# Optimization experiments

Measured on AMD Instinct MI355X. Metric: run time of the kernel, lower is better.

The kernel has to match this reference:

```python
import math
import jax, jax.numpy as jnp
import numpy as np

B, S, D, H = 4, 1024, 512, 8
DK = D // H


def lin(x, W, b):
    # torch nn.Linear: y = x @ W.T + b, W: [out, in]
    return jnp.einsum('...i,oi->...o', x, W) + b


def layer_norm(x, scale, bias, eps=1e-5):
    m = jnp.mean(x, axis=-1, keepdims=True)
    v = jnp.var(x, axis=-1, keepdims=True)
    return (x - m) / jnp.sqrt(v + eps) * scale + bias


def mha(q_in, k_in, v_in, Wq, bq, Wk, bk, Wv, bv, Wo, bo, gammas, mask, zero_pad):
    b, s, _ = q_in.shape
    q = lin(q_in, Wq, bq).reshape(b, s, H, DK).transpose(0, 2, 1, 3)  # bhsd
    k = lin(k_in, Wk, bk).reshape(b, s, H, DK).transpose(0, 2, 1, 3)
    v = lin(v_in, Wv, bv).reshape(b, s, H, DK).transpose(0, 2, 1, 3)
    scores = jnp.einsum('bhid,bhjd->bhij', q, k) / math.sqrt(DK)
    # no-grad distance-decay branch
    s_ = jnp.where(mask, scores, jnp.float32(-1e32))
    s_ = jax.nn.softmax(s_, axis=-1) * mask
    distcum = jnp.cumsum(s_, axis=-1)
    disttotal = jnp.sum(s_, axis=-1, keepdims=True)
    idx = jnp.arange(s)
    pos = jnp.abs(idx[None, :] - idx[:, None]).astype(jnp.float32)[None, None]  # |i-j|
    dist = jax.lax.stop_gradient(jnp.sqrt(jnp.clip((disttotal - distcum) * pos, 0.0, None)))
    gamma = -jax.nn.softplus(gammas)[None]  # [1,h,1,1]
    total_effect = jnp.clip(jnp.exp(dist * gamma), 1e-5, 1e5)
    scores = scores * total_effect
    # NOTE: original code calls scores.masked_fill(...) without assignment (no-op);
    # faithfully NOT re-masking before this softmax.
    att = jax.nn.softmax(scores, axis=-1)
    if zero_pad:
        att = att.at[:, :, 0, :].set(0.0)
    out = jnp.einsum('bhij,bhjd->bhid', att, v).transpose(0, 2, 1, 3).reshape(b, s, D)
    return lin(out, Wo, bo)


def setup_inputs() -> dict:
    key = jax.random.key(0)
    ks = jax.random.split(key, 32)
    ki = iter(range(32))

    def w(shape, scale=0.02):
        return jax.random.normal(ks[next(ki)], shape, jnp.float32) * scale

    inp = {
        'q_emb': jax.random.normal(ks[next(ki)], (B, S, D), jnp.float32),
        'qa_emb': jax.random.normal(ks[next(ki)], (B, S, D), jnp.float32),
    }
    for blk in (1, 2, 3):
        inp[f'Wq{blk}'] = w((D, D)); inp[f'bq{blk}'] = jnp.zeros((D,), jnp.float32)
        if blk == 3:
            inp['Wk3'] = w((D, D)); inp['bk3'] = jnp.zeros((D,), jnp.float32)
        inp[f'Wv{blk}'] = w((D, D)); inp[f'bv{blk}'] = jnp.zeros((D,), jnp.float32)
        inp[f'Wo{blk}'] = w((D, D)); inp[f'bo{blk}'] = jnp.zeros((D,), jnp.float32)
        inp[f'g{blk}'] = w((H, 1, 1), 0.5)
        inp[f'ls{blk}'] = jnp.ones((D,), jnp.float32)
        inp[f'lb{blk}'] = jnp.zeros((D,), jnp.float32)
    inp['know'] = jax.random.uniform(ks[next(ki)], (1, 1, D), jnp.float32, -1.0, 1.0)
    inp['Wlk'] = w((D, DK)); inp['b_lk'] = jnp.zeros((D,), jnp.float32)
    inp['Wlv'] = w((D, DK)); inp['b_lv'] = jnp.zeros((D,), jnp.float32)
    return inp


def reference(q_emb, qa_emb,
              Wq1, bq1, Wv1, bv1, Wo1, bo1, g1, ls1, lb1,
              Wq2, bq2, Wv2, bv2, Wo2, bo2, g2, ls2, lb2,
              Wq3, bq3, Wk3, bk3, Wv3, bv3, Wo3, bo3, g3, ls3, lb3,
              know, Wlk, b_lk, Wlv, b_lv):
    b, s, d = q_emb.shape
    ones = jnp.ones((s, s), dtype=bool)
    mask_peek = jnp.tril(ones, k=0)[None, None]   # peek_cur=True
    mask_nopeek = jnp.tril(ones, k=-1)[None, None]  # peek_cur=False

    # block1 / block2 share k and q projections (kq_same=True)
    hq = layer_norm(q_emb + mha(q_emb, q_emb, q_emb, Wq1, bq1, Wq1, bq1,
                                Wv1, bv1, Wo1, bo1, g1, mask_peek, False), ls1, lb1)
    ha = layer_norm(qa_emb + mha(qa_emb, qa_emb, qa_emb, Wq2, bq2, Wq2, bq2,
                                 Wv2, bv2, Wo2, bo2, g2, mask_peek, False), ls2, lb2)
    query = jnp.broadcast_to(know, (b, s, d))
    h = layer_norm(query + mha(query, hq, ha, Wq3, bq3, Wk3, bk3,
                               Wv3, bv3, Wo3, bo3, g3, mask_nopeek, True), ls3, lb3)

    # small multi-head combine
    key_t = jax.nn.sigmoid(lin(query.reshape(b, s, H, DK), Wlk, b_lk))  # [b,s,h,d]
    val_t = jax.nn.sigmoid(lin(h.reshape(b, s, H, DK), Wlv, b_lv))     # [b,s,h,d]
    beta = jnp.einsum('bshd,bsd->bsh', key_t, q_emb)
    alpha = jax.nn.softmax(beta, axis=-1)
    out = jnp.einsum('bsh,bshd->bsd', alpha, val_t)
    return out
```

## Files before the change

### kernel.cpp

```cpp
#include <hip/hip_runtime.h>
#include <math.h>

#define BB 4
#define S 1024
#define D 512
#define H 8
#define DKH 64

#define ATT_LD 1032
#define LOG2E 1.4426950408889634f

typedef __attribute__((ext_vector_type(8))) short bf16x8;
typedef __attribute__((ext_vector_type(4))) float f32x4;

#if __has_builtin(__builtin_amdgcn_exp2f)
#define EXP2(x) __builtin_amdgcn_exp2f(x)
#else
#define EXP2(x) exp2f(x)
#endif
#if __has_builtin(__builtin_amdgcn_sqrtf)
#define SQRTF(x) __builtin_amdgcn_sqrtf(x)
#else
#define SQRTF(x) sqrtf(x)
#endif
#if __has_builtin(__builtin_amdgcn_rcpf)
#define RCPF(x) __builtin_amdgcn_rcpf(x)
#else
#define RCPF(x) (1.0f / (x))
#endif

__device__ __forceinline__ unsigned short f2bf(float f){
  unsigned int u = __float_as_uint(f);
  u += 0x7FFFu + ((u >> 16) & 1u);
  return (unsigned short)(u >> 16);
}
__device__ __forceinline__ unsigned short f2bf_rhu(float f){
  return (unsigned short)((__float_as_uint(f) + 0x8000u) >> 16);
}
__device__ __forceinline__ unsigned int pk_rhu(float lo, float hi){
  unsigned int a = __float_as_uint(lo) + 0x8000u;
  unsigned int b = __float_as_uint(hi) + 0x8000u;
#if __has_builtin(__builtin_amdgcn_perm)
  return __builtin_amdgcn_perm(b, a, 0x07060302u);
#else
  return (a >> 16) | (b & 0xffff0000u);
#endif
}
__device__ __forceinline__ float bf2f(unsigned int v){
  return __uint_as_float(v << 16);
}
__device__ __forceinline__ f32x4 MFMA(bf16x8 a, bf16x8 b, f32x4 c){
  return __builtin_amdgcn_mfma_f32_16x16x32_bf16(a, b, c, 0, 0, 0);
}
__device__ __forceinline__ void gl_lds16(const void* g, void* l){
  __builtin_amdgcn_global_load_lds(
      (const __attribute__((address_space(1))) void*)g,
      (__attribute__((address_space(3))) void*)l, 16, 0, 0);
}

template<int CTRL>
__device__ __forceinline__ float dppadd(float v){
  int s = __builtin_amdgcn_update_dpp(0, __float_as_int(v), CTRL, 0xf, 0xf, true);
  return v + __int_as_float(s);
}
__device__ __forceinline__ float rdl(float v, int l){
  return __int_as_float(__builtin_amdgcn_readlane(__float_as_int(v), l));
}
__device__ __forceinline__ void wave_scan64(float v, int lane, float& incl, float& total){
  float r = dppadd<0x111>(v);
  r = dppadd<0x112>(r);
  r = dppadd<0x114>(r);
  r = dppadd<0x118>(r);
  float t0 = rdl(r, 15), t1 = rdl(r, 31), t2 = rdl(r, 47), t3 = rdl(r, 63);
  const int row = lane >> 4;
  float off = (row > 0 ? t0 : 0.f) + (row > 1 ? t1 : 0.f) + (row > 2 ? t2 : 0.f);
  incl = r + off;
  total = (t0 + t1) + (t2 + t3);
}
__device__ __forceinline__ float wave_sum64(float v){
  float r = dppadd<0x111>(v);
  r = dppadd<0x112>(r);
  r = dppadd<0x114>(r);
  r = dppadd<0x118>(r);
  return (rdl(r, 15) + rdl(r, 31)) + (rdl(r, 47) + rdl(r, 63));
}

__device__ __forceinline__ float blk_sum(float* r, int t, float v){
  r[t] = v; __syncthreads();
  for (int s = 128; s > 0; s >>= 1){
    if (t < s) r[t] += r[t + s];
    __syncthreads();
  }
  float res = r[0]; __syncthreads();
  return res;
}

struct GemmJobs {
  const unsigned short* A[4];
  const unsigned short* W[4];
  const float* bias[4];
  void* C[4];
};
template<int OUTBF>
__global__ __launch_bounds__(256) void mfma_gemm_b(GemmJobs jb)
{
  __shared__ __align__(16) short As[128][32];
  __shared__ __align__(16) short Ws[128][32];
  const int t = threadIdx.x;
  const int z = blockIdx.z;
  const int n0 = blockIdx.x * 128, m0 = blockIdx.y * 128;
  const unsigned short* A = jb.A[z];
  const unsigned short* W = jb.W[z];
  const float* bias = jb.bias[z];
  const int w = t >> 6, lane = t & 63;
  const int wm = (w >> 1) << 6, wn = (w & 1) << 6;
  const int lm = lane & 15, q = lane >> 4;
  const int r = t >> 2, cc = (t & 3) << 3;
  char* ldsA = ((char*)&As[0][0]) + w * 1024;
  char* ldsW = ((char*)&Ws[0][0]) + w * 1024;
  f32x4 acc[4][4];
  #pragma unroll
  for (int a_ = 0; a_ < 4; a_++)
    #pragma unroll
    for (int b_ = 0; b_ < 4; b_++)
      acc[a_][b_] = (f32x4){0.f, 0.f, 0.f, 0.f};
  for (int k0 = 0; k0 < D; k0 += 32){
    gl_lds16(&A[(size_t)(m0 + r)      * D + k0 + cc], ldsA);
    gl_lds16(&A[(size_t)(m0 + r + 64) * D + k0 + cc], ldsA + 4096);
    gl_lds16(&W[(size_t)(n0 + r)      * D + k0 + cc], ldsW);
    gl_lds16(&W[(size_t)(n0 + r + 64) * D + k0 + cc], ldsW + 4096);
    __syncthreads();
    bf16x8 af[4], bf[4];
    #pragma unroll
    for (int mt = 0; mt < 4; mt++) af[mt] = *(const bf16x8*)&As[wm + mt*16 + lm][q*8];
    #pragma unroll
    for (int nt = 0; nt < 4; nt++) bf[nt] = *(const bf16x8*)&Ws[wn + nt*16 + lm][q*8];
    #pragma unroll
    for (int mt = 0; mt < 4; mt++)
      #pragma unroll
      for (int nt = 0; nt < 4; nt++)
        acc[mt][nt] = MFMA(af[mt], bf[nt], acc[mt][nt]);
    __syncthreads();
  }
  #pragma unroll
  for (int nt = 0; nt < 4; nt++){
    const int n = n0 + wn + nt*16 + lm;
    const float bs = bias[n];
    #pragma unroll
    for (int mt = 0; mt < 4; mt++){
      const int mb = m0 + wm + mt*16 + (q << 2);
      f32x4 c = acc[mt][nt];
      #pragma unroll
      for (int rr = 0; rr < 4; rr++){
        float vv = c[rr] + bs;
        if (OUTBF)
          ((unsigned short*)jb.C[z])[(size_t)(mb + rr) * D + n] = f2bf(vv);
        else
          ((float*)jb.C[z])[(size_t)(mb + rr) * D + n] = vv;
      }
    }
  }
}

#define KS_LD 66
struct VTArgs { const unsigned short* v[2]; unsigned short* vt[2]; };
__global__ __launch_bounds__(256) void vt_kernel(VTArgs a)
{
  __shared__ unsigned short tile[64 * KS_LD];
  const int z = blockIdx.z, bh = blockIdx.y, b = bh >> 3, h = bh & 7;
  const int j0 = blockIdx.x * 64;
  const int t = threadIdx.x;
  const unsigned short* vp = a.v[z];
  unsigned short* vtp = a.vt[z] + (size_t)bh * 64 * S;
  #pragma unroll
  for (int p = 0; p < 2; p++){
    int lin = t + p * 256, row = lin >> 3, c8 = (lin & 7) << 3;
    *(uint4*)&tile[row * KS_LD + c8] =
      *(const uint4*)&vp[((size_t)b * S + j0 + row) * D + h * DKH + c8];
  }
  __syncthreads();
  #pragma unroll
  for (int p = 0; p < 2; p++){
    int lin = t + p * 256, d = lin >> 3, c8 = (lin & 7) << 3;
    unsigned short tmp[8];
    #pragma unroll
    for (int jx = 0; jx < 8; jx++) tmp[jx] = tile[(c8 + jx) * KS_LD + d];
    *(uint4*)&vtp[(size_t)d * S + j0 + c8] = *(const uint4*)tmp;
  }
}

struct FAArgs {
  const unsigned short* qk[2];
  const unsigned short* vt[2];
  unsigned short* ctx[2];
  const float* g[2];
  const float* c3;
  int diag, zero_pad;
};
template<int C3>
__global__ __launch_bounds__(256, 4) void fused_attn(FAArgs a)
{
  __shared__ __align__(16) unsigned short att[16 * ATT_LD];
  __shared__ float ls2s[16];
  const int t = threadIdx.x;
  const int z = blockIdx.z;
  const int bh = blockIdx.y, b = bh >> 3, h = bh & 7;
  const int i0 = blockIdx.x * 16;
  const int w = t >> 6, lane = t & 63, lm = lane & 15, q = lane >> 4;
  const unsigned short* qkp = a.qk[z];
  const unsigned short* vtp = a.vt[z] + (size_t)bh * 64 * S;
  unsigned short* ctxp = a.ctx[z];
  float gm2;
  { float gv = a.g[z][h];
    gm2 = -((gv > 20.f) ? gv : log1pf(expf(gv))) * LOG2E; }

  if (!C3){
    const size_t rowbase = (size_t)b * S;
    bf16x8 af0 = *(const bf16x8*)&qkp[(rowbase + i0 + lm) * D + h * DKH + q*8];
    bf16x8 af1 = *(const bf16x8*)&qkp[(rowbase + i0 + lm) * D + h * DKH + 32 + q*8];
    size_t kb = (rowbase + w*16 + lm) * D + h * DKH;
    bf16x8 bv0 = *(const bf16x8*)&qkp[kb + q*8];
    bf16x8 bv1 = *(const bf16x8*)&qkp[kb + 32 + q*8];
    for (int jc = 0; jc < S; jc += 64){
      bf16x8 nb0, nb1;
      if (jc + 64 < S){
        size_t kb2 = (rowbase + jc + 64 + w*16 + lm) * D + h * DKH;
        nb0 = *(const bf16x8*)&qkp[kb2 + q*8];
        nb1 = *(const bf16x8*)&qkp[kb2 + 32 + q*8];
      }
      f32x4 acc = (f32x4){0.f, 0.f, 0.f, 0.f};
      acc = MFMA(af0, bv0, acc);
      acc = MFMA(af1, bv1, acc);
      #pragma unroll
      for (int rr = 0; rr < 4; rr++)
        att[(q*4 + rr) * ATT_LD + jc + w*16 + lm] = f2bf_rhu(acc[rr] * 0.125f);
      bv0 = nb0; bv1 = nb1;
    }
  }
  __syncthreads();

  const int jA0 = lane * 8, jB0 = 512 + lane * 8;

  float cH[16], erH[16];
  if (C3){
    const float* c3p = a.c3 + ((size_t)b * H + h) * S;
    #pragma unroll
    for (int sg = 0; sg < 2; sg++)
      #pragma unroll
      for (int p4 = 0; p4 < 2; p4++){
        float4 x = *(const float4*)&c3p[sg*512 + lane*8 + p4*4];
        cH[sg*8+p4*4+0] = x.x * LOG2E; cH[sg*8+p4*4+1] = x.y * LOG2E;
        cH[sg*8+p4*4+2] = x.z * LOG2E; cH[sg*8+p4*4+3] = x.w * LOG2E;
      }
    #pragma unroll
    for (int k = 0; k < 16; k++) erH[k] = EXP2(cH[k]);
  }

  auto decay_row = [&](const float (&c)[16], const float (&er)[16],
                       const int i, unsigned short* rowp, const int rl){
    const int jmax = i + a.diag;
    const bool skipB = (jmax < 512);
    float pl[16];
    float runA = 0.f;
    #pragma unroll
    for (int k = 0; k < 8; k++){
      float e = (jA0 + k <= jmax) ? er[k] : 0.f;
      runA += e; pl[k] = runA;
    }
    float sA, TA;
    wave_scan64(runA, lane, sA, TA);
    float T = TA, sB = 0.f, runB = 0.f;
    if (!skipB){
      #pragma unroll
      for (int k = 0; k < 8; k++){
        float e = (jB0 + k <= jmax) ? er[8+k] : 0.f;
        runB += e; pl[8+k] = runB;
      }
      float TB;
      wave_scan64(runB, lane, sB, TB);
      T = TA + TB;
    }
    const float inv1 = RCPF(T);
    const float cbaseA = (T - (sA - runA)) * inv1;
    const float fiA = (float)(i - jA0);
    float ls2 = 0.f;
    #pragma unroll
    for (int k = 0; k < 8; k++){
      float remn = fmaf(-pl[k], inv1, cbaseA);
      float pos  = fabsf(fiA - (float)k);
      float dist = SQRTF(fmaxf(remn * pos, 0.f));
      float eff  = fmaxf(EXP2(gm2 * dist), 1e-5f);
      float pp   = EXP2(c[k] * eff);
      ls2 += pp; pl[k] = pp;
    }
    if (!skipB){
      const float cbaseB = (T - (TA + sB - runB)) * inv1;
      const float fiB = (float)(i - jB0);
      #pragma unroll
      for (int k = 0; k < 8; k++){
        float remn = fmaf(-pl[8+k], inv1, cbaseB);
        float pos  = fabsf(fiB - (float)k);
        float dist = SQRTF(fmaxf(remn * pos, 0.f));
        float eff  = fmaxf(EXP2(gm2 * dist), 1e-5f);
        float pp   = EXP2(c[8+k] * eff);
        ls2 += pp; pl[8+k] = pp;
      }
    } else {
      #pragma unroll
      for (int k = 0; k < 8; k++){ pl[8+k] = er[8+k]; ls2 += er[8+k]; }
    }
    ls2 = wave_sum64(ls2);
    if (lane == 0) ls2s[rl] = RCPF(ls2);
    #pragma unroll
    for (int sg = 0; sg < 2; sg++){
      uint4 o;
      o.x = pk_rhu(pl[sg*8+0], pl[sg*8+1]);
      o.y = pk_rhu(pl[sg*8+2], pl[sg*8+3]);
      o.z = pk_rhu(pl[sg*8+4], pl[sg*8+5]);
      o.w = pk_rhu(pl[sg*8+6], pl[sg*8+7]);
      *(uint4*)&rowp[sg*512 + lane*8] = o;
    }
  };

  for (int rloc = 0; rloc < 4; rloc++){
    const int rl = w*4 + rloc;
    const int i = i0 + rl;
    unsigned short* rowp = &att[rl * ATT_LD];
    if (C3 && a.zero_pad && i == 0){
      uint4 zz = make_uint4(0u,0u,0u,0u);
      *(uint4*)&rowp[jA0] = zz;
      *(uint4*)&rowp[jB0] = zz;
      if (lane == 0) ls2s[0] = 1.f;
      continue;
    }
    if (C3){
      decay_row(cH, erH, i, rowp, rl);
    } else {
      float c[16], er[16];
      #pragma unroll
      for (int sg = 0; sg < 2; sg++){
        uint4 u = *(const uint4*)&rowp[sg*512 + lane*8];
        unsigned int uu[4] = {u.x, u.y, u.z, u.w};
        #pragma unroll
        for (int mel = 0; mel < 4; mel++){
          c[sg*8 + mel*2]     = bf2f(uu[mel] & 0xffffu) * LOG2E;
          c[sg*8 + mel*2 + 1] = bf2f(uu[mel] >> 16) * LOG2E;
        }
      }
      #pragma unroll
      for (int k = 0; k < 16; k++) er[k] = EXP2(c[k]);
      decay_row(c, er, i, rowp, rl);
    }
  }
  __syncthreads();

  f32x4 acc = (f32x4){0.f,0.f,0.f,0.f};
  const unsigned short* vrow = &vtp[(size_t)(w*16 + lm) * S];
  bf16x8 bv0 = *(const bf16x8*)&vrow[q*8];
  bf16x8 bv1 = *(const bf16x8*)&vrow[32 + q*8];
  for (int kc = 0; kc < S; kc += 64){
    bf16x8 nb0, nb1;
    if (kc + 64 < S){
      nb0 = *(const bf16x8*)&vrow[kc + 64 + q*8];
      nb1 = *(const bf16x8*)&vrow[kc + 96 + q*8];
    }
    bf16x8 a0 = *(const bf16x8*)&att[lm * ATT_LD + kc + q*8];
    bf16x8 a1 = *(const bf16x8*)&att[lm * ATT_LD + kc + 32 + q*8];
    acc = MFMA(a0, bv0, acc);
    acc = MFMA(a1, bv1, acc);
    bv0 = nb0; bv1 = nb1;
  }
  #pragma unroll
  for (int rr = 0; rr < 4; rr++){
    const int rl = q*4 + rr;
    const float sc = ls2s[rl];
    const int row = i0 + rl;
    ctxp[((size_t)b * S + row) * D + h * DKH + w*16 + lm] = f2bf(acc[rr] * sc);
  }
}

struct LNJobs {
  const float* resid[2];
  const float* y[2];
  const float* ls[2];
  const float* lb[2];
  unsigned short* out[2];
  int bcast[2];
};
__global__ __launch_bounds__(256) void ln_residual_b(LNJobs j)
{
  const int z = blockIdx.y;
  const int r = blockIdx.x, t = threadIdx.x;
  __shared__ float red[256];
  const size_t base = (size_t)r * D;
  const float* resid = j.resid[z];
  const float* y = j.y[z];
  const int bcast = j.bcast[z];
  float r0 = bcast ? resid[t]       : resid[base + t];
  float r1 = bcast ? resid[t + 256] : resid[base + t + 256];
  float x0 = r0 + y[base + t];
  float x1 = r1 + y[base + t + 256];
  float mean = blk_sum(red, t, x0 + x1) * (1.0f / 512.0f);
  float d0 = x0 - mean, d1 = x1 - mean;
  float var = blk_sum(red, t, d0*d0 + d1*d1) * (1.0f / 512.0f);
  float inv = rsqrtf(var + 1e-5f);
  j.out[z][base + t]       = f2bf(d0 * inv * j.ls[z][t]       + j.lb[z][t]);
  j.out[z][base + t + 256] = f2bf(d1 * inv * j.ls[z][t + 256] + j.lb[z][t + 256]);
}

struct CvtJobs {
  const float* s[12];
  unsigned short* d[12];
  int n[12];
};
__global__ __launch_bounds__(256) void cvt_all(CvtJobs jb){
  const int z = blockIdx.y;
  const int n = jb.n[z];
  const float* s = jb.s[z];
  unsigned short* d = jb.d[z];
  for (int idx = blockIdx.x * 256 + threadIdx.x; idx < n; idx += gridDim.x * 256)
    d[idx] = f2bf(s[idx]);
}

__global__ __launch_bounds__(256) void know_kernel(
    const float* __restrict__ know, const float* __restrict__ Wq3,
    const float* __restrict__ bq3, float* __restrict__ q3,
    const float* __restrict__ Wlk, const float* __restrict__ blk_,
    float* __restrict__ keyt)
{
  if (blockIdx.x < 128){
    const int wv = (blockIdx.x * 256 + threadIdx.x) >> 6;
    const int lane = threadIdx.x & 63;
    const float* wr = Wq3 + (size_t)wv * 512 + lane * 8;
    const float* kr = know + lane * 8;
    float4 w0 = *(const float4*)&wr[0], w1 = *(const float4*)&wr[4];
    float4 k0 = *(const float4*)&kr[0], k1 = *(const float4*)&kr[4];
    float p = w0.x*k0.x + w0.y*k0.y + w0.z*k0.z + w0.w*k0.w
            + w1.x*k1.x + w1.y*k1.y + w1.z*k1.z + w1.w*k1.w;
    p = wave_sum64(p);
    if (lane == 0) q3[wv] = p + bq3[wv];
  } else {
    int idx = (blockIdx.x - 128) * 256 + threadIdx.x;
    int h = idx >> 9, n = idx & 511;
    float acc = 0.f;
    for (int i = 0; i < 64; i++) acc += know[h * 64 + i] * Wlk[(size_t)n * 64 + i];
    keyt[idx] = 1.f / (1.f + __expf(-(acc + blk_[n])));
  }
}

__global__ __launch_bounds__(256) void scores3_kernel(
    const float* __restrict__ q3, const unsigned short* __restrict__ k3,
    float* __restrict__ c3)
{
  int idx = blockIdx.x * 256 + threadIdx.x;
  int j  = idx & (S - 1);
  int bh = idx >> 10;
  int h  = bh & 7, b = bh >> 3;
  const unsigned short* kp = k3 + ((size_t)b * S + j) * D + h * DKH;
  const float* qp = q3 + h * DKH;
  float acc = 0.f;
  #pragma unroll
  for (int d8 = 0; d8 < 64; d8 += 8){
    uint4 u = *(const uint4*)&kp[d8];
    unsigned int uu[4] = {u.x, u.y, u.z, u.w};
    #pragma unroll
    for (int mel = 0; mel < 4; mel++){
      acc += qp[d8 + 2*mel]     * bf2f(uu[mel] & 0xffffu);
      acc += qp[d8 + 2*mel + 1] * bf2f(uu[mel] >> 16);
    }
  }
  c3[idx] = acc * 0.125f;
}

__global__ __launch_bounds__(256) void alphas_kernel(
    const float* __restrict__ keyt, const float* __restrict__ q_emb,
    float* __restrict__ alpha)
{
  const int row = blockIdx.x * 4 + (threadIdx.x >> 6);
  const int l = threadIdx.x & 63;
  const int h = l >> 3, sub = l & 7;
  const float* qr = q_emb + (size_t)row * D;
  const float* kt = keyt + h * D;
  float p = 0.f;
  for (int d = sub; d < D; d += 8) p += kt[d] * qr[d];
  p += __shfl_xor(p, 1, 64);
  p += __shfl_xor(p, 2, 64);
  p += __shfl_xor(p, 4, 64);
  float m = p;
  m = fmaxf(m, __shfl_xor(m, 8, 64));
  m = fmaxf(m, __shfl_xor(m, 16, 64));
  m = fmaxf(m, __shfl_xor(m, 32, 64));
  float e = __expf(p - m);
  float ssum = e;
  ssum += __shfl_xor(ssum, 8, 64);
  ssum += __shfl_xor(ssum, 16, 64);
  ssum += __shfl_xor(ssum, 32, 64);
  if (sub == 0) alpha[(size_t)row * H + h] = e / ssum;
}

__global__ __launch_bounds__(256) void val_fused(
    const unsigned short* __restrict__ Ah,
    const unsigned short* __restrict__ Wv,
    const float* __restrict__ blv,
    const float* __restrict__ alpha,
    float* __restrict__ out)
{
  __shared__ __align__(16) short As[128][32];
  __shared__ __align__(16) short Ws[128][32];
  __shared__ float als[128];
  const int t = threadIdx.x;
  const int n0 = blockIdx.x * 128, m0 = blockIdx.y * 128;
  if (t < 128) als[t] = alpha[m0 + t];
  const int w = t >> 6, lane = t & 63;
  const int wm = (w >> 1) << 6, wn = (w & 1) << 6;
  const int lm = lane & 15, q = lane >> 4;
  const int r = t >> 2, cc = (t & 3) << 3;
  f32x4 acc[4][4];
  #pragma unroll
  for (int a_ = 0; a_ < 4; a_++)
    #pragma unroll
    for (int b_ = 0; b_ < 4; b_++)
      acc[a_][b_] = (f32x4){0.f, 0.f, 0.f, 0.f};
  for (int k0 = 0; k0 < 64; k0 += 32){
    *(uint4*)&As[r][cc]      = *(const uint4*)&Ah[(size_t)(m0 + r) * 64 + k0 + cc];
    *(uint4*)&As[r + 64][cc] = *(const uint4*)&Ah[(size_t)(m0 + r + 64) * 64 + k0 + cc];
    *(uint4*)&Ws[r][cc]      = *(const uint4*)&Wv[(size_t)(n0 + r) * 64 + k0 + cc];
    *(uint4*)&Ws[r + 64][cc] = *(const uint4*)&Wv[(size_t)(n0 + r + 64) * 64 + k0 + cc];
    __syncthreads();
    bf16x8 af[4], bf[4];
    #pragma unroll
    for (int mt = 0; mt < 4; mt++) af[mt] = *(const bf16x8*)&As[wm + mt*16 + lm][q*8];
    #pragma unroll
    for (int nt = 0; nt < 4; nt++) bf[nt] = *(const bf16x8*)&Ws[wn + nt*16 + lm][q*8];
    #pragma unroll
    for (int mt = 0; mt < 4; mt++)
      #pragma unroll
      for (int nt = 0; nt < 4; nt++)
        acc[mt][nt] = MFMA(af[mt], bf[nt], acc[mt][nt]);
    __syncthreads();
  }
  #pragma unroll
  for (int nt = 0; nt < 4; nt++){
    const int n = n0 + wn + nt*16 + lm;
    const float bs = blv[n];
    #pragma unroll
    for (int mt = 0; mt < 4; mt++){
      const int mb = m0 + wm + mt*16;
      f32x4 c = acc[mt][nt];
      float part = 0.f;
      #pragma unroll
      for (int rr = 0; rr < 4; rr++){
        const int ml = (mb - m0) + (q << 2) + rr;
        float sg = 1.f / (1.f + __expf(-(c[rr] + bs)));
        part += als[ml] * sg;
      }
      part += __shfl_xor(part, 16, 64);
      if ((q & 1) == 0){
        const int srow = (mb >> 3) + (q >> 1);
        out[(size_t)srow * D + n] = part;
      }
    }
  }
}

extern "C" void kernel_launch(void* const* d_in, const int* in_sizes, int n_in,
                              void* d_out, int out_size, void* d_ws, size_t ws_size,
                              hipStream_t stream) {
  const float* q_emb  = (const float*)d_in[0];
  const float* qa_emb = (const float*)d_in[1];
  const float* Wq1 = (const float*)d_in[2],  *bq1 = (const float*)d_in[3];
  const float* Wv1 = (const float*)d_in[4],  *bv1 = (const float*)d_in[5];
  const float* Wo1 = (const float*)d_in[6],  *bo1 = (const float*)d_in[7];
  const float* g1  = (const float*)d_in[8],  *ls1 = (const float*)d_in[9],  *lb1 = (const float*)d_in[10];
  const float* Wq2 = (const float*)d_in[11], *bq2 = (const float*)d_in[12];
  const float* Wv2 = (const float*)d_in[13], *bv2 = (const float*)d_in[14];
  const float* Wo2 = (const float*)d_in[15], *bo2 = (const float*)d_in[16];
  const float* g2  = (const float*)d_in[17], *ls2 = (const float*)d_in[18], *lb2 = (const float*)d_in[19];
  const float* Wq3 = (const float*)d_in[20], *bq3 = (const float*)d_in[21];
  const float* Wk3 = (const float*)d_in[22], *bk3 = (const float*)d_in[23];
  const float* Wv3 = (const float*)d_in[24], *bv3 = (const float*)d_in[25];
  const float* Wo3 = (const float*)d_in[26], *bo3 = (const float*)d_in[27];
  const float* g3  = (const float*)d_in[28], *ls3 = (const float*)d_in[29], *lb3 = (const float*)d_in[30];
  const float* know = (const float*)d_in[31];
  const float* Wlk  = (const float*)d_in[32], *b_lk = (const float*)d_in[33];
  const float* Wlv  = (const float*)d_in[34], *b_lv = (const float*)d_in[35];
  float* outp = (float*)d_out;

  const size_t NSD = (size_t)BB * S * D;
  unsigned short* p = (unsigned short*)d_ws;
  unsigned short* qk1b = p; p += NSD;
  unsigned short* v1b  = p; p += NSD;
  unsigned short* qk2b = p; p += NSD;
  unsigned short* v2b  = p; p += NSD;
  unsigned short* k3b  = p; p += NSD;
  unsigned short* v3b  = p; p += NSD;
  unsigned short* ctx1b= p; p += NSD;
  unsigned short* ctx2b= p; p += NSD;
  unsigned short* ctx3b= p; p += NSD;
  unsigned short* xqb  = p; p += NSD;
  unsigned short* xab  = p; p += NSD;
  unsigned short* hqb  = p; p += NSD;
  unsigned short* hab  = p; p += NSD;
  unsigned short* hfb  = p; p += NSD;
  unsigned short* vt1  = p; p += NSD;
  unsigned short* vt2  = p; p += NSD;
  unsigned short* vt3  = p; p += NSD;
  unsigned short* wb   = p; p += (size_t)9 * D * D;
  unsigned short* wlvb = p; p += (size_t)D * DKH;
  float* yv0   = (float*)p;
  float* yv1   = yv0 + NSD;
  float* q3    = yv1 + NSD;
  float* keyt  = q3 + 512;
  float* c3    = keyt + 4096;
  float* alpha = c3 + (size_t)BB * H * S;

  unsigned short* Wq1b = wb + 0*(size_t)D*D;
  unsigned short* Wv1b = wb + 1*(size_t)D*D;
  unsigned short* Wo1b = wb + 2*(size_t)D*D;
  unsigned short* Wq2b = wb + 3*(size_t)D*D;
  unsigned short* Wv2b = wb + 4*(size_t)D*D;
  unsigned short* Wo2b = wb + 5*(size_t)D*D;
  unsigned short* Wk3b = wb + 6*(size_t)D*D;
  unsigned short* Wv3b = wb + 7*(size_t)D*D;
  unsigned short* Wo3b = wb + 8*(size_t)D*D;

  CvtJobs jb;
  jb.s[0] = q_emb;  jb.d[0] = xqb;  jb.n[0] = (int)NSD;
  jb.s[1] = qa_emb; jb.d[1] = xab;  jb.n[1] = (int)NSD;
  jb.s[2] = Wq1; jb.d[2] = Wq1b; jb.n[2] = D*D;
  jb.s[3] = Wv1; jb.d[3] = Wv1b; jb.n[3] = D*D;
  jb.s[4] = Wo1; jb.d[4] = Wo1b; jb.n[4] = D*D;
  jb.s[5] = Wq2; jb.d[5] = Wq2b; jb.n[5] = D*D;
  jb.s[6] = Wv2; jb.d[6] = Wv2b; jb.n[6] = D*D;
  jb.s[7] = Wo2; jb.d[7] = Wo2b; jb.n[7] = D*D;
  jb.s[8] = Wk3; jb.d[8] = Wk3b; jb.n[8] = D*D;
  jb.s[9] = Wv3; jb.d[9] = Wv3b; jb.n[9] = D*D;
  jb.s[10] = Wo3; jb.d[10] = Wo3b; jb.n[10] = D*D;
  jb.s[11] = Wlv; jb.d[11] = wlvb; jb.n[11] = D*DKH;
  cvt_all<<<dim3(256, 12), 256, 0, stream>>>(jb);

  {
    GemmJobs g;
    g.A[0]=xqb; g.W[0]=Wq1b; g.bias[0]=bq1; g.C[0]=qk1b;
    g.A[1]=xqb; g.W[1]=Wv1b; g.bias[1]=bv1; g.C[1]=v1b;
    g.A[2]=xab; g.W[2]=Wq2b; g.bias[2]=bq2; g.C[2]=qk2b;
    g.A[3]=xab; g.W[3]=Wv2b; g.bias[3]=bv2; g.C[3]=v2b;
    mfma_gemm_b<1><<<dim3(4, 32, 4), 256, 0, stream>>>(g);
  }
  { VTArgs a; a.v[0]=v1b; a.v[1]=v2b; a.vt[0]=vt1; a.vt[1]=vt2;
    vt_kernel<<<dim3(16, 32, 2), 256, 0, stream>>>(a); }
  { FAArgs a;
    a.qk[0]=qk1b; a.qk[1]=qk2b; a.vt[0]=vt1; a.vt[1]=vt2;
    a.ctx[0]=ctx1b; a.ctx[1]=ctx2b; a.g[0]=g1; a.g[1]=g2;
    a.c3=nullptr; a.diag=0; a.zero_pad=0;
    fused_attn<0><<<dim3(64, 32, 2), 256, 0, stream>>>(a); }
  {
    GemmJobs g;
    g.A[0]=ctx1b; g.W[0]=Wo1b; g.bias[0]=bo1; g.C[0]=yv0;
    g.A[1]=ctx2b; g.W[1]=Wo2b; g.bias[1]=bo2; g.C[1]=yv1;
    g.A[2]=ctx1b; g.W[2]=Wo1b; g.bias[2]=bo1; g.C[2]=yv0;
    g.A[3]=ctx1b; g.W[3]=Wo1b; g.bias[3]=bo1; g.C[3]=yv0;
    mfma_gemm_b<0><<<dim3(4, 32, 2), 256, 0, stream>>>(g);
  }
  {
    LNJobs lj;
    lj.resid[0]=q_emb;  lj.y[0]=yv0; lj.ls[0]=ls1; lj.lb[0]=lb1; lj.out[0]=hqb; lj.bcast[0]=0;
    lj.resid[1]=qa_emb; lj.y[1]=yv1; lj.ls[1]=ls2; lj.lb[1]=lb2; lj.out[1]=hab; lj.bcast[1]=0;
    ln_residual_b<<<dim3(BB*S, 2), 256, 0, stream>>>(lj);
  }

  know_kernel<<<144, 256, 0, stream>>>(know, Wq3, bq3, q3, Wlk, b_lk, keyt);
  {
    GemmJobs g;
    g.A[0]=hqb; g.W[0]=Wk3b; g.bias[0]=bk3; g.C[0]=k3b;
    g.A[1]=hab; g.W[1]=Wv3b; g.bias[1]=bv3; g.C[1]=v3b;
    g.A[2]=hqb; g.W[2]=Wk3b; g.bias[2]=bk3; g.C[2]=k3b;
    g.A[3]=hqb; g.W[3]=Wk3b; g.bias[3]=bk3; g.C[3]=k3b;
    mfma_gemm_b<1><<<dim3(4, 32, 2), 256, 0, stream>>>(g);
  }
  { VTArgs a; a.v[0]=v3b; a.v[1]=v3b; a.vt[0]=vt3; a.vt[1]=vt3;
    vt_kernel<<<dim3(16, 32, 1), 256, 0, stream>>>(a); }
  scores3_kernel<<<128, 256, 0, stream>>>(q3, k3b, c3);
  { FAArgs a;
    a.qk[0]=k3b; a.qk[1]=k3b; a.vt[0]=vt3; a.vt[1]=vt3;
    a.ctx[0]=ctx3b; a.ctx[1]=ctx3b; a.g[0]=g3; a.g[1]=g3;
    a.c3=c3; a.diag=-1; a.zero_pad=1;
    fused_attn<1><<<dim3(64, 32, 1), 256, 0, stream>>>(a); }
  {
    GemmJobs g;
    g.A[0]=ctx3b; g.W[0]=Wo3b; g.bias[0]=bo3; g.C[0]=yv0;
    g.A[1]=ctx3b; g.W[1]=Wo3b; g.bias[1]=bo3; g.C[1]=yv0;
    g.A[2]=ctx3b; g.W[2]=Wo3b; g.bias[2]=bo3; g.C[2]=yv0;
    g.A[3]=ctx3b; g.W[3]=Wo3b; g.bias[3]=bo3; g.C[3]=yv0;
    mfma_gemm_b<0><<<dim3(4, 32, 1), 256, 0, stream>>>(g);
  }
  {
    LNJobs lj;
    lj.resid[0]=know; lj.y[0]=yv0; lj.ls[0]=ls3; lj.lb[0]=lb3; lj.out[0]=hfb; lj.bcast[0]=1;
    lj.resid[1]=know; lj.y[1]=yv0; lj.ls[1]=ls3; lj.lb[1]=lb3; lj.out[1]=hfb; lj.bcast[1]=1;
    ln_residual_b<<<dim3(BB*S, 1), 256, 0, stream>>>(lj);
  }

  alphas_kernel<<<1024, 256, 0, stream>>>(keyt, q_emb, alpha);
  val_fused<<<dim3(4, 256), 256, 0, stream>>>(hfb, wlvb, b_lv, alpha, outp);
}
```

Measured before the change: 430.3 us.

## Double fused attention block to 512 threads with split-K PV reduction

The fused attention kernel now runs 8 waves per block instead of 4. Each wave handles two score rows instead of four, the QK score tiles are strided across 8 waves, and the P·V product is split along the key dimension, with the two halves combined through shared memory. The softmax normalisation is folded into the probabilities before they are packed to bf16, which removes the per-row scale array. This aims to cut the serial per-row decay work per wave and raise latency hiding, at the cost of extra barriers, a shared-memory reduction, and register pressure under the new launch bounds.

New measurement: 438.0 us. No clear change (+1.8%).

```diff
diff --git a/kernel.cpp b/kernel.cpp
--- a/kernel.cpp
+++ b/kernel.cpp
@@ -198,10 +198,9 @@
   int diag, zero_pad;
 };
 template<int C3>
-__global__ __launch_bounds__(256, 4) void fused_attn(FAArgs a)
+__global__ __launch_bounds__(512, 8) void fused_attn(FAArgs a)
 {
   __shared__ __align__(16) unsigned short att[16 * ATT_LD];
-  __shared__ float ls2s[16];
   const int t = threadIdx.x;
   const int z = blockIdx.z;
   const int bh = blockIdx.y, b = bh >> 3, h = bh & 7;
@@ -221,10 +220,11 @@
     size_t kb = (rowbase + w*16 + lm) * D + h * DKH;
     bf16x8 bv0 = *(const bf16x8*)&qkp[kb + q*8];
     bf16x8 bv1 = *(const bf16x8*)&qkp[kb + 32 + q*8];
-    for (int jc = 0; jc < S; jc += 64){
+    for (int it = 0; it < 8; it++){
+      const int cb = it*128 + w*16;
       bf16x8 nb0, nb1;
-      if (jc + 64 < S){
-        size_t kb2 = (rowbase + jc + 64 + w*16 + lm) * D + h * DKH;
+      if (it < 7){
+        size_t kb2 = (rowbase + cb + 128 + lm) * D + h * DKH;
         nb0 = *(const bf16x8*)&qkp[kb2 + q*8];
         nb1 = *(const bf16x8*)&qkp[kb2 + 32 + q*8];
       }
@@ -233,7 +233,7 @@
       acc = MFMA(af1, bv1, acc);
       #pragma unroll
       for (int rr = 0; rr < 4; rr++)
-        att[(q*4 + rr) * ATT_LD + jc + w*16 + lm] = f2bf_rhu(acc[rr] * 0.125f);
+        att[(q*4 + rr) * ATT_LD + cb + lm] = f2bf_rhu(acc[rr] * 0.125f);
       bv0 = nb0; bv1 = nb1;
     }
   }
@@ -257,7 +257,7 @@
   }
 
   auto decay_row = [&](const float (&c)[16], const float (&er)[16],
-                       const int i, unsigned short* rowp, const int rl){
+                       const int i, unsigned short* rowp){
     const int jmax = i + a.diag;
     const bool skipB = (jmax < 512);
     float pl[16];
@@ -310,31 +310,31 @@
       for (int k = 0; k < 8; k++){ pl[8+k] = er[8+k]; ls2 += er[8+k]; }
     }
     ls2 = wave_sum64(ls2);
-    if (lane == 0) ls2s[rl] = RCPF(ls2);
+    const float inv2 = RCPF(ls2);
     #pragma unroll
     for (int sg = 0; sg < 2; sg++){
       uint4 o;
-      o.x = pk_rhu(pl[sg*8+0], pl[sg*8+1]);
-      o.y = pk_rhu(pl[sg*8+2], pl[sg*8+3]);
-      o.z = pk_rhu(pl[sg*8+4], pl[sg*8+5]);
-      o.w = pk_rhu(pl[sg*8+6], pl[sg*8+7]);
+      o.x = pk_rhu(pl[sg*8+0]*inv2, pl[sg*8+1]*inv2);
+      o.y = pk_rhu(pl[sg*8+2]*inv2, pl[sg*8+3]*inv2);
+      o.z = pk_rhu(pl[sg*8+4]*inv2, pl[sg*8+5]*inv2);
+      o.w = pk_rhu(pl[sg*8+6]*inv2, pl[sg*8+7]*inv2);
       *(uint4*)&rowp[sg*512 + lane*8] = o;
     }
   };
 
-  for (int rloc = 0; rloc < 4; rloc++){
-    const int rl = w*4 + rloc;
+  #pragma unroll
+  for (int rloc = 0; rloc < 2; rloc++){
+    const int rl = w*2 + rloc;
     const int i = i0 + rl;
     unsigned short* rowp = &att[rl * ATT_LD];
     if (C3 && a.zero_pad && i == 0){
       uint4 zz = make_uint4(0u,0u,0u,0u);
       *(uint4*)&rowp[jA0] = zz;
       *(uint4*)&rowp[jB0] = zz;
-      if (lane == 0) ls2s[0] = 1.f;
       continue;
     }
     if (C3){
-      decay_row(cH, erH, i, rowp, rl);
+      decay_row(cH, erH, i, rowp);
     } else {
       float c[16], er[16];
       #pragma unroll
@@ -349,18 +349,19 @@
       }
       #pragma unroll
       for (int k = 0; k < 16; k++) er[k] = EXP2(c[k]);
-      decay_row(c, er, i, rowp, rl);
+      decay_row(c, er, i, rowp);
     }
   }
   __syncthreads();
 
+  const int ct = w & 3, kc0 = (w >> 2) * 512;
   f32x4 acc = (f32x4){0.f,0.f,0.f,0.f};
-  const unsigned short* vrow = &vtp[(size_t)(w*16 + lm) * S];
-  bf16x8 bv0 = *(const bf16x8*)&vrow[q*8];
-  bf16x8 bv1 = *(const bf16x8*)&vrow[32 + q*8];
-  for (int kc = 0; kc < S; kc += 64){
+  const unsigned short* vrow = &vtp[(size_t)(ct*16 + lm) * S];
+  bf16x8 bv0 = *(const bf16x8*)&vrow[kc0 + q*8];
+  bf16x8 bv1 = *(const bf16x8*)&vrow[kc0 + 32 + q*8];
+  for (int kc = kc0; kc < kc0 + 512; kc += 64){
     bf16x8 nb0, nb1;
-    if (kc + 64 < S){
+    if (kc + 64 < kc0 + 512){
       nb0 = *(const bf16x8*)&vrow[kc + 64 + q*8];
       nb1 = *(const bf16x8*)&vrow[kc + 96 + q*8];
     }
@@ -370,12 +371,21 @@
     acc = MFMA(a1, bv1, acc);
     bv0 = nb0; bv1 = nb1;
   }
-  #pragma unroll
-  for (int rr = 0; rr < 4; rr++){
-    const int rl = q*4 + rr;
-    const float sc = ls2s[rl];
-    const int row = i0 + rl;
-    ctxp[((size_t)b * S + row) * D + h * DKH + w*16 + lm] = f2bf(acc[rr] * sc);
+  __syncthreads();
+  float* red = (float*)att;
+  if (w >= 4){
+    #pragma unroll
+    for (int rr = 0; rr < 4; rr++)
+      red[(q*4 + rr) * 68 + ct*16 + lm] = acc[rr];
+  }
+  __syncthreads();
+  if (w < 4){
+    #pragma unroll
+    for (int rr = 0; rr < 4; rr++){
+      const float v = acc[rr] + red[(q*4 + rr) * 68 + ct*16 + lm];
+      const int row = i0 + q*4 + rr;
+      ctxp[((size_t)b * S + row) * D + h * DKH + ct*16 + lm] = f2bf(v);
+    }
   }
 }
 
@@ -653,7 +663,7 @@
     a.qk[0]=qk1b; a.qk[1]=qk2b; a.vt[0]=vt1; a.vt[1]=vt2;
     a.ctx[0]=ctx1b; a.ctx[1]=ctx2b; a.g[0]=g1; a.g[1]=g2;
     a.c3=nullptr; a.diag=0; a.zero_pad=0;
-    fused_attn<0><<<dim3(64, 32, 2), 256, 0, stream>>>(a); }
+    fused_attn<0><<<dim3(64, 32, 2), 512, 0, stream>>>(a); }
   {
     GemmJobs g;
     g.A[0]=ctx1b; g.W[0]=Wo1b; g.bias[0]=bo1; g.C[0]=yv0;
@@ -685,7 +695,7 @@
     a.qk[0]=k3b; a.qk[1]=k3b; a.vt[0]=vt3; a.vt[1]=vt3;
     a.ctx[0]=ctx3b; a.ctx[1]=ctx3b; a.g[0]=g3; a.g[1]=g3;
     a.c3=c3; a.diag=-1; a.zero_pad=1;
-    fused_attn<1><<<dim3(64, 32, 1), 256, 0, stream>>>(a); }
+    fused_attn<1><<<dim3(64, 32, 1), 512, 0, stream>>>(a); }
   {
     GemmJobs g;
     g.A[0]=ctx3b; g.W[0]=Wo3b; g.bias[0]=bo3; g.C[0]=yv0;
```
